# Performance work log

Measured on AMD Instinct MI355X. Metric: run time of the kernel, lower is better.

The kernel has to match this reference:

```python
import jax, jax.numpy as jnp
import numpy as np

N = 100000   # nodes
E = 1600000  # edges
C = 128      # channels
EPS = 1e-5   # BatchNorm eps (PyG gnn.BatchNorm default)


def gcn_conv(x, W, b, src, dst, n):
    """PyG GCNConv: linear -> sym-normalized aggregation with self-loops -> bias."""
    h = x @ W                                      # [N, C]
    # degree with self-loops: in-degree at dst + 1
    deg = jnp.zeros((n,), h.dtype).at[dst].add(jnp.ones((), h.dtype)) + 1.0
    dinv = jax.lax.rsqrt(deg)                      # [N]
    norm = dinv[src] * dinv[dst]                   # [E]
    agg = jnp.zeros_like(h).at[dst].add(h[src] * norm[:, None])
    agg = agg + h * (dinv * dinv)[:, None]         # self-loop contribution
    return agg + b


def batch_norm(x, gamma, beta):
    """Training-mode BatchNorm over the node dimension (per-channel)."""
    mu = jnp.mean(x, axis=0)
    var = jnp.mean(jnp.square(x - mu), axis=0)     # biased variance
    return (x - mu) * jax.lax.rsqrt(var + EPS) * gamma + beta


def setup_inputs() -> dict:
    key = jax.random.key(0)
    ks = jax.random.split(key, 8)
    s = 1.0 / np.sqrt(C)
    x = jax.random.normal(ks[0], (N, C), dtype=jnp.float32)
    edge_index = jax.random.randint(ks[1], (2, E), 0, N, dtype=jnp.int64)
    W1 = jax.random.uniform(ks[2], (C, C), jnp.float32, -s, s)
    b1 = jax.random.uniform(ks[3], (C,), jnp.float32, -s, s)
    W2 = jax.random.uniform(ks[4], (C, C), jnp.float32, -s, s)
    b2 = jax.random.uniform(ks[5], (C,), jnp.float32, -s, s)
    gamma2 = jnp.ones((C,), jnp.float32)
    beta2 = jnp.zeros((C,), jnp.float32)
    return {"x": x, "W1": W1, "b1": b1, "W2": W2, "b2": b2,
            "gamma2": gamma2, "beta2": beta2, "edge_index": edge_index}


def reference(x, W1, b1, W2, b2, gamma2, beta2, edge_index):
    src, dst = edge_index[0], edge_index[1]
    identity = x
    # NOTE: original forward applies batch_norm2 after BOTH convs (batch_norm1 unused).
    h = jax.nn.relu(batch_norm(gcn_conv(x, W1, b1, src, dst, N), gamma2, beta2))
    h = batch_norm(gcn_conv(h, W2, b2, src, dst, N), gamma2, beta2)
    return jax.nn.relu(h + identity)
```

## Files before the change

kernel.cpp:

```cpp
#include <hip/hip_runtime.h>

#define N_NODES 100000
#define EDGES   1600000
#define CH      128
#define BN_EPS  1e-5f

#define BINS     782
#define CHUNKS   128
#define CHUNK_E  (EDGES / CHUNKS)
#define HM       (BINS * CHUNKS)
#define SCAN_NB  (HM / 256)
#define NREP     64

typedef __attribute__((ext_vector_type(8))) __bf16 bf16x8;
typedef __attribute__((ext_vector_type(4))) __bf16 bf16x4;
typedef __attribute__((ext_vector_type(2))) __bf16 bf16x2;
typedef __attribute__((ext_vector_type(4))) float  f32x4;

__global__ __launch_bounds__(256) void histo_kernel(const int* __restrict__ dst,
                                                    int* __restrict__ histo_g) {
    __shared__ int h[BINS];
    int t = threadIdx.x;
    for (int b = t; b < BINS; b += 256) h[b] = 0;
    __syncthreads();
    int base = blockIdx.x * CHUNK_E;
    for (int i = t; i < CHUNK_E; i += 256)
        atomicAdd(&h[dst[base + i] >> 7], 1);
    __syncthreads();
    for (int b = t; b < BINS; b += 256)
        histo_g[b * CHUNKS + blockIdx.x] = h[b];
}

__global__ __launch_bounds__(256) void scan1(const int* __restrict__ in,
                                             int* __restrict__ scanned,
                                             int* __restrict__ blocksum) {
    __shared__ int sh[2][256];
    int t = threadIdx.x;
    int i = blockIdx.x * 256 + t;
    int v = in[i];
    sh[0][t] = v;
    __syncthreads();
    int pp = 0;
    #pragma unroll
    for (int off = 1; off < 256; off <<= 1) {
        int val = sh[pp][t] + ((t >= off) ? sh[pp][t - off] : 0);
        sh[1 - pp][t] = val;
        pp = 1 - pp;
        __syncthreads();
    }
    int incl = sh[pp][t];
    scanned[i] = incl - v;
    if (t == 255) blocksum[blockIdx.x] = incl;
}

__global__ __launch_bounds__(512) void scan2(int* __restrict__ blocksum) {
    __shared__ int sh[2][512];
    int t = threadIdx.x;
    int v = (t < SCAN_NB) ? blocksum[t] : 0;
    sh[0][t] = v;
    __syncthreads();
    int pp = 0;
    #pragma unroll
    for (int off = 1; off < 512; off <<= 1) {
        int val = sh[pp][t] + ((t >= off) ? sh[pp][t - off] : 0);
        sh[1 - pp][t] = val;
        pp = 1 - pp;
        __syncthreads();
    }
    if (t < SCAN_NB) blocksum[t] = sh[pp][t] - v;
}

__global__ __launch_bounds__(256) void scan3(int* __restrict__ scanned,
                                             const int* __restrict__ blocksum) {
    int i = blockIdx.x * 256 + threadIdx.x;
    scanned[i] += blocksum[blockIdx.x];
    if (i == HM - 1) scanned[HM] = EDGES;
}

__global__ __launch_bounds__(256) void place_kernel(const int* __restrict__ src,
                                                    const int* __restrict__ dst,
                                                    const int* __restrict__ scanned,
                                                    int* __restrict__ binned) {
    __shared__ int cur[BINS];
    int t = threadIdx.x;
    for (int b = t; b < BINS; b += 256)
        cur[b] = scanned[b * CHUNKS + blockIdx.x];
    __syncthreads();
    int base = blockIdx.x * CHUNK_E;
    for (int i = t; i < CHUNK_E; i += 256) {
        int d = dst[base + i];
        int s = src[base + i];
        int pos = atomicAdd(&cur[d >> 7], 1);
        binned[pos] = (s << 7) | (d & 127);
    }
}

__global__ __launch_bounds__(256) void bin_csr(const int* __restrict__ binned,
                                               const int* __restrict__ scanned,
                                               int* __restrict__ srcs,
                                               int* __restrict__ rowptr,
                                               float* __restrict__ dinv) {
    __shared__ int cnt[128];
    __shared__ int sc[2][128];
    __shared__ int base[128];
    __shared__ int cur[128];
    const int t = threadIdx.x;
    const int bin = blockIdx.x;
    if (t < 128) { cnt[t] = 0; cur[t] = 0; }
    __syncthreads();
    const int beg = scanned[bin * CHUNKS];
    const int end = scanned[bin * CHUNKS + CHUNKS];
    for (int e = beg + t; e < end; e += 256)
        atomicAdd(&cnt[binned[e] & 127], 1);
    __syncthreads();
    if (t < 128) sc[0][t] = cnt[t];
    __syncthreads();
    int pp = 0;
    #pragma unroll
    for (int off = 1; off < 128; off <<= 1) {
        if (t < 128) sc[1 - pp][t] = sc[pp][t] + ((t >= off) ? sc[pp][t - off] : 0);
        pp = 1 - pp;
        __syncthreads();
    }
    if (t < 128) {
        base[t] = beg + sc[pp][t] - cnt[t];
        int n = (bin << 7) + t;
        if (n < N_NODES) {
            rowptr[n] = base[t];
            dinv[n] = rsqrtf((float)cnt[t] + 1.0f);
        }
    }
    if (bin == 0 && t == 0) rowptr[N_NODES] = EDGES;
    __syncthreads();
    for (int e = beg + t; e < end; e += 256) {
        int p = binned[e];
        int dl = p & 127;
        int pos = base[dl] + atomicAdd(&cur[dl], 1);
        srcs[pos] = p >> 7;
    }
}

__global__ __launch_bounds__(256) void wtrans(const float* __restrict__ W,
                                              __bf16* __restrict__ Wt) {
    int idx = blockIdx.x * 256 + threadIdx.x;
    int n = idx >> 7, k = idx & 127;
    Wt[idx] = (__bf16)W[k * 128 + n];
}

__global__ __launch_bounds__(256) void gemm_f32(const float* __restrict__ A,
                                                const __bf16* __restrict__ Wt,
                                                const float* __restrict__ dinv,
                                                __bf16* __restrict__ hs) {
    const int wave = threadIdx.x >> 6;
    const int rt = blockIdx.x * 4 + wave;
    if (rt >= N_NODES / 16) return;
    const int lane = threadIdx.x & 63;
    const int ln = lane & 15;
    const int quad = lane >> 4;
    const int arow = rt * 16 + ln;

    f32x4 acc[8];
    #pragma unroll
    for (int ct = 0; ct < 8; ++ct) acc[ct] = (f32x4){0.f, 0.f, 0.f, 0.f};

    #pragma unroll
    for (int k0 = 0; k0 < 128; k0 += 32) {
        const int k = k0 + quad * 8;
        float4 a0 = *(const float4*)(A + (size_t)arow * CH + k);
        float4 a1 = *(const float4*)(A + (size_t)arow * CH + k + 4);
        bf16x8 af;
        af[0] = (__bf16)a0.x; af[1] = (__bf16)a0.y;
        af[2] = (__bf16)a0.z; af[3] = (__bf16)a0.w;
        af[4] = (__bf16)a1.x; af[5] = (__bf16)a1.y;
        af[6] = (__bf16)a1.z; af[7] = (__bf16)a1.w;
        #pragma unroll
        for (int ct = 0; ct < 8; ++ct) {
            bf16x8 bfrag = *(const bf16x8*)(Wt + (size_t)(ct * 16 + ln) * CH + k);
            acc[ct] = __builtin_amdgcn_mfma_f32_16x16x32_bf16(af, bfrag, acc[ct], 0, 0, 0);
        }
    }

    #pragma unroll
    for (int r = 0; r < 4; ++r) {
        const int row_r = rt * 16 + quad * 4 + r;
        const float dr = dinv[row_r];
        __bf16* orow = hs + (size_t)row_r * CH + ln;
        #pragma unroll
        for (int ct = 0; ct < 8; ++ct)
            orow[ct * 16] = (__bf16)(acc[ct][r] * dr);
    }
}

__global__ __launch_bounds__(256) void gemm_bn(const __bf16* __restrict__ A,
                                               const __bf16* __restrict__ Wt,
                                               const float* __restrict__ dinv,
                                               const float* __restrict__ scale,
                                               const float* __restrict__ shift,
                                               __bf16* __restrict__ hs) {
    const int wave = threadIdx.x >> 6;
    const int rt = blockIdx.x * 4 + wave;
    if (rt >= N_NODES / 16) return;
    const int lane = threadIdx.x & 63;
    const int ln = lane & 15;
    const int quad = lane >> 4;
    const int arow = rt * 16 + ln;

    f32x4 acc[8];
    #pragma unroll
    for (int ct = 0; ct < 8; ++ct) acc[ct] = (f32x4){0.f, 0.f, 0.f, 0.f};

    #pragma unroll
    for (int k0 = 0; k0 < 128; k0 += 32) {
        const int k = k0 + quad * 8;
        bf16x8 av = *(const bf16x8*)(A + (size_t)arow * CH + k);
        bf16x8 af;
        #pragma unroll
        for (int j = 0; j < 8; ++j)
            af[j] = (__bf16)fmaxf(fmaf((float)av[j], scale[k + j], shift[k + j]), 0.f);
        #pragma unroll
        for (int ct = 0; ct < 8; ++ct) {
            bf16x8 bfrag = *(const bf16x8*)(Wt + (size_t)(ct * 16 + ln) * CH + k);
            acc[ct] = __builtin_amdgcn_mfma_f32_16x16x32_bf16(af, bfrag, acc[ct], 0, 0, 0);
        }
    }

    #pragma unroll
    for (int r = 0; r < 4; ++r) {
        const int row_r = rt * 16 + quad * 4 + r;
        const float dr = dinv[row_r];
        __bf16* orow = hs + (size_t)row_r * CH + ln;
        #pragma unroll
        for (int ct = 0; ct < 8; ++ct)
            orow[ct * 16] = (__bf16)(acc[ct][r] * dr);
    }
}

__global__ __launch_bounds__(256) void gather_agg(const __bf16* __restrict__ hs,
                                                  const int* __restrict__ srcs,
                                                  const int* __restrict__ rowptr,
                                                  const float* __restrict__ dinv,
                                                  __bf16* __restrict__ agg,
                                                  float* __restrict__ gpart) {
    __shared__ float red[4][64][4];
    const int wave = threadIdx.x >> 6;
    const int n = __builtin_amdgcn_readfirstlane(blockIdx.x * 4 + wave);
    const int c2 = threadIdx.x & 63;
    int beg = rowptr[n];
    int end = rowptr[n + 1];
    const bf16x2* hp = (const bf16x2*)hs;
    bf16x2 sv = hp[(size_t)n * 64 + c2];
    float ax = (float)sv[0], ay = (float)sv[1];
    int j = beg;
    for (; j + 8 <= end; j += 8) {
        int s0 = srcs[j + 0], s1 = srcs[j + 1], s2 = srcs[j + 2], s3 = srcs[j + 3];
        int s4 = srcs[j + 4], s5 = srcs[j + 5], s6 = srcs[j + 6], s7 = srcs[j + 7];
        bf16x2 v0 = hp[(size_t)s0 * 64 + c2];
        bf16x2 v1 = hp[(size_t)s1 * 64 + c2];
        bf16x2 v2 = hp[(size_t)s2 * 64 + c2];
        bf16x2 v3 = hp[(size_t)s3 * 64 + c2];
        bf16x2 v4 = hp[(size_t)s4 * 64 + c2];
        bf16x2 v5 = hp[(size_t)s5 * 64 + c2];
        bf16x2 v6 = hp[(size_t)s6 * 64 + c2];
        bf16x2 v7 = hp[(size_t)s7 * 64 + c2];
        ax += (((float)v0[0] + (float)v1[0]) + ((float)v2[0] + (float)v3[0]))
            + (((float)v4[0] + (float)v5[0]) + ((float)v6[0] + (float)v7[0]));
        ay += (((float)v0[1] + (float)v1[1]) + ((float)v2[1] + (float)v3[1]))
            + (((float)v4[1] + (float)v5[1]) + ((float)v6[1] + (float)v7[1]));
    }
    for (; j < end; ++j) {
        bf16x2 v = hp[(size_t)srcs[j] * 64 + c2];
        ax += (float)v[0];
        ay += (float)v[1];
    }
    float d = dinv[n];
    float ox = ax * d, oy = ay * d;
    bf16x2 o; o[0] = (__bf16)ox; o[1] = (__bf16)oy;
    ((bf16x2*)agg)[(size_t)n * 64 + c2] = o;

    f32x4 rv; rv[0] = ox; rv[1] = ox * ox; rv[2] = oy; rv[3] = oy * oy;
    *(f32x4*)red[wave][c2] = rv;
    __syncthreads();
    const int t = threadIdx.x;
    float v = red[0][t >> 2][t & 3] + red[1][t >> 2][t & 3] +
              red[2][t >> 2][t & 3] + red[3][t >> 2][t & 3];
    atomicAdd(&gpart[(blockIdx.x & (NREP - 1)) * 256 + t], v);
}

__global__ void bn_final(const float* __restrict__ gpart,
                         const float* __restrict__ gamma,
                         const float* __restrict__ beta,
                         float* __restrict__ scale,
                         float* __restrict__ shift) {
    int c = threadIdx.x;
    int c2 = c >> 1, odd = c & 1;
    float s = 0.f, ss = 0.f;
    for (int r = 0; r < NREP; ++r) {
        s  += gpart[r * 256 + c2 * 4 + 2 * odd];
        ss += gpart[r * 256 + c2 * 4 + 2 * odd + 1];
    }
    const float invN = 1.0f / (float)N_NODES;
    float mu = s * invN;
    float var = ss * invN - mu * mu;
    float sc = gamma[c] * rsqrtf(var + BN_EPS);
    scale[c] = sc;
    shift[c] = beta[c] - mu * sc;
}

__global__ __launch_bounds__(256) void bn_apply_res_relu(const __bf16* __restrict__ v,
                                                         const float* __restrict__ scale,
                                                         const float* __restrict__ shift,
                                                         const float* __restrict__ xin,
                                                         float* __restrict__ outv) {
    int i = blockIdx.x * 256 + threadIdx.x;
    int cg = i & 31;
    bf16x4 a4 = ((const bf16x4*)v)[i];
    float4 r = ((const float4*)xin)[i];
    float4 sc = ((const float4*)scale)[cg];
    float4 sh = ((const float4*)shift)[cg];
    float4 a;
    a.x = fmaxf(fmaf((float)a4[0], sc.x, sh.x) + r.x, 0.f);
    a.y = fmaxf(fmaf((float)a4[1], sc.y, sh.y) + r.y, 0.f);
    a.z = fmaxf(fmaf((float)a4[2], sc.z, sh.z) + r.z, 0.f);
    a.w = fmaxf(fmaf((float)a4[3], sc.w, sh.w) + r.w, 0.f);
    ((float4*)outv)[i] = a;
}

extern "C" void kernel_launch(void* const* d_in, const int* in_sizes, int n_in,
                              void* d_out, int out_size, void* d_ws, size_t ws_size,
                              hipStream_t stream) {
    const float* x      = (const float*)d_in[0];
    const float* W1     = (const float*)d_in[1];
    const float* W2     = (const float*)d_in[3];
    const float* gamma2 = (const float*)d_in[5];
    const float* beta2  = (const float*)d_in[6];
    const int*   ei     = (const int*)d_in[7];
    const int*   srcI   = ei;
    const int*   dstI   = ei + EDGES;
    float* out = (float*)d_out;

    char* ws = (char*)d_ws;
    __bf16* agg      = (__bf16*)(ws);
    __bf16* hs       = (__bf16*)(ws + 25600000);
    int*    binned   = (int*)   (ws + 51200000);
    int*    srcs     = (int*)   (ws + 57600000);
    int*    histo_g  = (int*)   (ws + 64000000);
    int*    scanned  = (int*)   (ws + 64400512);
    int*    blocksum = (int*)   (ws + 64801024);
    float*  dinv     = (float*) (ws + 64802688);
    int*    rowptr   = (int*)   (ws + 65202688);
    __bf16* Wt1      = (__bf16*)(ws + 65602816);
    __bf16* Wt2      = (__bf16*)(ws + 65635584);
    float*  gpart    = (float*) (ws + 65668352);
    float*  scale1   = (float*) (ws + 65733888);
    float*  shift1   = scale1 + 128;
    float*  scale2   = scale1 + 256;
    float*  shift2   = scale1 + 384;

    const int ELEM4_BLOCKS = (N_NODES * 32) / 256;
    const int GEMM_BLOCKS  = (N_NODES / 16 + 3) / 4;
    const int NODE4_BLOCKS = N_NODES / 4;

    histo_kernel<<<CHUNKS, 256, 0, stream>>>(dstI, histo_g);
    scan1<<<SCAN_NB, 256, 0, stream>>>(histo_g, scanned, blocksum);
    scan2<<<1, 512, 0, stream>>>(blocksum);
    scan3<<<SCAN_NB, 256, 0, stream>>>(scanned, blocksum);
    place_kernel<<<CHUNKS, 256, 0, stream>>>(srcI, dstI, scanned, binned);
    bin_csr<<<BINS, 256, 0, stream>>>(binned, scanned, srcs, rowptr, dinv);
    wtrans<<<64, 256, 0, stream>>>(W1, Wt1);
    wtrans<<<64, 256, 0, stream>>>(W2, Wt2);

    gemm_f32<<<GEMM_BLOCKS, 256, 0, stream>>>(x, Wt1, dinv, hs);
    hipMemsetAsync(gpart, 0, NREP * 256 * sizeof(float), stream);
    gather_agg<<<NODE4_BLOCKS, 256, 0, stream>>>(hs, srcs, rowptr, dinv, agg, gpart);
    bn_final<<<1, 128, 0, stream>>>(gpart, gamma2, beta2, scale1, shift1);

    gemm_bn<<<GEMM_BLOCKS, 256, 0, stream>>>(agg, Wt2, dinv, scale1, shift1, hs);
    hipMemsetAsync(gpart, 0, NREP * 256 * sizeof(float), stream);
    gather_agg<<<NODE4_BLOCKS, 256, 0, stream>>>(hs, srcs, rowptr, dinv, agg, gpart);
    bn_final<<<1, 128, 0, stream>>>(gpart, gamma2, beta2, scale2, shift2);
    bn_apply_res_relu<<<ELEM4_BLOCKS, 256, 0, stream>>>(agg, scale2, shift2, x, out);
}
```

Before: 403.4 us.

## Gather 16-byte rows with 4 edges per wave, 4 nodes per wave

The gather kernel now has each lane load 8 bf16 channels (16 bytes) instead of 2. A wave covers four edges at once in four lane groups, then combines them with cross-lane shuffles. Each wave processes four nodes in sequence and keeps BN partial sums in registers, which cuts block count and atomic traffic by 4x. The two weight-transpose launches are merged into one. The aim is fewer, wider memory transactions and more edges in flight per wave. The cost is extra shuffle work, more registers, and less parallelism when node degrees vary.

```diff
diff --git a/kernel.cpp b/kernel.cpp
--- a/kernel.cpp
+++ b/kernel.cpp
@@ -140,9 +140,14 @@
     }
 }
 
-__global__ __launch_bounds__(256) void wtrans(const float* __restrict__ W,
-                                              __bf16* __restrict__ Wt) {
-    int idx = blockIdx.x * 256 + threadIdx.x;
+__global__ __launch_bounds__(256) void wtrans2(const float* __restrict__ W1,
+                                               __bf16* __restrict__ Wt1,
+                                               const float* __restrict__ W2,
+                                               __bf16* __restrict__ Wt2) {
+    int b = blockIdx.x;
+    const float* W = (b < 64) ? W1 : W2;
+    __bf16* Wt = (b < 64) ? Wt1 : Wt2;
+    int idx = (b & 63) * 256 + threadIdx.x;
     int n = idx >> 7, k = idx & 127;
     Wt[idx] = (__bf16)W[k * 128 + n];
 }
@@ -241,48 +246,87 @@
                                                   const float* __restrict__ dinv,
                                                   __bf16* __restrict__ agg,
                                                   float* __restrict__ gpart) {
-    __shared__ float red[4][64][4];
+    __shared__ float red[4][256];
     const int wave = threadIdx.x >> 6;
-    const int n = __builtin_amdgcn_readfirstlane(blockIdx.x * 4 + wave);
-    const int c2 = threadIdx.x & 63;
-    int beg = rowptr[n];
-    int end = rowptr[n + 1];
-    const bf16x2* hp = (const bf16x2*)hs;
-    bf16x2 sv = hp[(size_t)n * 64 + c2];
-    float ax = (float)sv[0], ay = (float)sv[1];
-    int j = beg;
-    for (; j + 8 <= end; j += 8) {
-        int s0 = srcs[j + 0], s1 = srcs[j + 1], s2 = srcs[j + 2], s3 = srcs[j + 3];
-        int s4 = srcs[j + 4], s5 = srcs[j + 5], s6 = srcs[j + 6], s7 = srcs[j + 7];
-        bf16x2 v0 = hp[(size_t)s0 * 64 + c2];
-        bf16x2 v1 = hp[(size_t)s1 * 64 + c2];
-        bf16x2 v2 = hp[(size_t)s2 * 64 + c2];
-        bf16x2 v3 = hp[(size_t)s3 * 64 + c2];
-        bf16x2 v4 = hp[(size_t)s4 * 64 + c2];
-        bf16x2 v5 = hp[(size_t)s5 * 64 + c2];
-        bf16x2 v6 = hp[(size_t)s6 * 64 + c2];
-        bf16x2 v7 = hp[(size_t)s7 * 64 + c2];
-        ax += (((float)v0[0] + (float)v1[0]) + ((float)v2[0] + (float)v3[0]))
-            + (((float)v4[0] + (float)v5[0]) + ((float)v6[0] + (float)v7[0]));
-        ay += (((float)v0[1] + (float)v1[1]) + ((float)v2[1] + (float)v3[1]))
-            + (((float)v4[1] + (float)v5[1]) + ((float)v6[1] + (float)v7[1]));
-    }
-    for (; j < end; ++j) {
-        bf16x2 v = hp[(size_t)srcs[j] * 64 + c2];
-        ax += (float)v[0];
-        ay += (float)v[1];
-    }
-    float d = dinv[n];
-    float ox = ax * d, oy = ay * d;
-    bf16x2 o; o[0] = (__bf16)ox; o[1] = (__bf16)oy;
-    ((bf16x2*)agg)[(size_t)n * 64 + c2] = o;
-
-    f32x4 rv; rv[0] = ox; rv[1] = ox * ox; rv[2] = oy; rv[3] = oy * oy;
-    *(f32x4*)red[wave][c2] = rv;
+    const int lane = threadIdx.x & 63;
+    const int lg = lane & 15;
+    const int eg = lane >> 4;
+    const bf16x8* hp8 = (const bf16x8*)hs;
+
+    float sstat[8], sstat2[8];
+    #pragma unroll
+    for (int i = 0; i < 8; ++i) { sstat[i] = 0.f; sstat2[i] = 0.f; }
+
+    for (int it = 0; it < 4; ++it) {
+        const int n = __builtin_amdgcn_readfirstlane(blockIdx.x * 16 + wave * 4 + it);
+        const int beg = rowptr[n];
+        const int end = rowptr[n + 1];
+
+        bf16x8 sv = hp8[(size_t)n * 16 + lg];
+        float acc[8];
+        #pragma unroll
+        for (int i = 0; i < 8; ++i) acc[i] = (eg == 0) ? (float)sv[i] : 0.f;
+
+        int j = beg;
+        for (; j + 16 <= end; j += 16) {
+            int s0 = srcs[j + eg];
+            int s1 = srcs[j + 4 + eg];
+            int s2 = srcs[j + 8 + eg];
+            int s3 = srcs[j + 12 + eg];
+            bf16x8 v0 = hp8[(size_t)s0 * 16 + lg];
+            bf16x8 v1 = hp8[(size_t)s1 * 16 + lg];
+            bf16x8 v2 = hp8[(size_t)s2 * 16 + lg];
+            bf16x8 v3 = hp8[(size_t)s3 * 16 + lg];
+            #pragma unroll
+            for (int i = 0; i < 8; ++i)
+                acc[i] += (((float)v0[i] + (float)v1[i]) +
+                           ((float)v2[i] + (float)v3[i]));
+        }
+        for (; j + 4 <= end; j += 4) {
+            int s = srcs[j + eg];
+            bf16x8 v = hp8[(size_t)s * 16 + lg];
+            #pragma unroll
+            for (int i = 0; i < 8; ++i) acc[i] += (float)v[i];
+        }
+        if (j < end) {
+            int idx = j + eg;
+            if (idx < end) {
+                int s = srcs[idx];
+                bf16x8 v = hp8[(size_t)s * 16 + lg];
+                #pragma unroll
+                for (int i = 0; i < 8; ++i) acc[i] += (float)v[i];
+            }
+        }
+
+        #pragma unroll
+        for (int i = 0; i < 8; ++i) {
+            acc[i] += __shfl_xor(acc[i], 16, 64);
+            acc[i] += __shfl_xor(acc[i], 32, 64);
+        }
+
+        const float d = dinv[n];
+        bf16x8 o;
+        #pragma unroll
+        for (int i = 0; i < 8; ++i) {
+            float ox = acc[i] * d;
+            o[i] = (__bf16)ox;
+            sstat[i] += ox;
+            sstat2[i] += ox * ox;
+        }
+        if (eg == 0)
+            ((bf16x8*)agg)[(size_t)n * 16 + lg] = o;
+    }
+
+    if (eg == 0) {
+        #pragma unroll
+        for (int i = 0; i < 8; ++i) {
+            red[wave][lg * 16 + i]     = sstat[i];
+            red[wave][lg * 16 + 8 + i] = sstat2[i];
+        }
+    }
     __syncthreads();
     const int t = threadIdx.x;
-    float v = red[0][t >> 2][t & 3] + red[1][t >> 2][t & 3] +
-              red[2][t >> 2][t & 3] + red[3][t >> 2][t & 3];
+    float v = red[0][t] + red[1][t] + red[2][t] + red[3][t];
     atomicAdd(&gpart[(blockIdx.x & (NREP - 1)) * 256 + t], v);
 }
 
@@ -292,11 +336,11 @@
                          float* __restrict__ scale,
                          float* __restrict__ shift) {
     int c = threadIdx.x;
-    int c2 = c >> 1, odd = c & 1;
+    int lg = c >> 3, i = c & 7;
     float s = 0.f, ss = 0.f;
     for (int r = 0; r < NREP; ++r) {
-        s  += gpart[r * 256 + c2 * 4 + 2 * odd];
-        ss += gpart[r * 256 + c2 * 4 + 2 * odd + 1];
+        s  += gpart[r * 256 + lg * 16 + i];
+        ss += gpart[r * 256 + lg * 16 + 8 + i];
     }
     const float invN = 1.0f / (float)N_NODES;
     float mu = s * invN;
@@ -358,7 +402,7 @@
 
     const int ELEM4_BLOCKS = (N_NODES * 32) / 256;
     const int GEMM_BLOCKS  = (N_NODES / 16 + 3) / 4;
-    const int NODE4_BLOCKS = N_NODES / 4;
+    const int GATHER_BLOCKS = N_NODES / 16;
 
     histo_kernel<<<CHUNKS, 256, 0, stream>>>(dstI, histo_g);
     scan1<<<SCAN_NB, 256, 0, stream>>>(histo_g, scanned, blocksum);
@@ -366,17 +410,16 @@
     scan3<<<SCAN_NB, 256, 0, stream>>>(scanned, blocksum);
     place_kernel<<<CHUNKS, 256, 0, stream>>>(srcI, dstI, scanned, binned);
     bin_csr<<<BINS, 256, 0, stream>>>(binned, scanned, srcs, rowptr, dinv);
-    wtrans<<<64, 256, 0, stream>>>(W1, Wt1);
-    wtrans<<<64, 256, 0, stream>>>(W2, Wt2);
+    wtrans2<<<128, 256, 0, stream>>>(W1, Wt1, W2, Wt2);
 
     gemm_f32<<<GEMM_BLOCKS, 256, 0, stream>>>(x, Wt1, dinv, hs);
     hipMemsetAsync(gpart, 0, NREP * 256 * sizeof(float), stream);
-    gather_agg<<<NODE4_BLOCKS, 256, 0, stream>>>(hs, srcs, rowptr, dinv, agg, gpart);
+    gather_agg<<<GATHER_BLOCKS, 256, 0, stream>>>(hs, srcs, rowptr, dinv, agg, gpart);
     bn_final<<<1, 128, 0, stream>>>(gpart, gamma2, beta2, scale1, shift1);
 
     gemm_bn<<<GEMM_BLOCKS, 256, 0, stream>>>(agg, Wt2, dinv, scale1, shift1, hs);
     hipMemsetAsync(gpart, 0, NREP * 256 * sizeof(float), stream);
-    gather_agg<<<NODE4_BLOCKS, 256, 0, stream>>>(hs, srcs, rowptr, dinv, agg, gpart);
+    gather_agg<<<GATHER_BLOCKS, 256, 0, stream>>>(hs, srcs, rowptr, dinv, agg, gpart);
     bn_final<<<1, 128, 0, stream>>>(gpart, gamma2, beta2, scale2, shift2);
     bn_apply_res_relu<<<ELEM4_BLOCKS, 256, 0, stream>>>(agg, scale2, shift2, x, out);
 }
```

Result: slower. 419.9 us (+4.1%).
